# Kernel optimization log

Measured on AMD Instinct MI355X. Metric: run time of the kernel, lower is better.

The kernel has to match this reference:

```python
import jax, jax.numpy as jnp
import numpy as np

# TT-factorized linear: 784 = 7*4*7*4 -> 512 = 4*4*8*4, max_rank=20
# canonical TT ranks: [1, 20, 20, 16, 1] (r3 capped by m4*n4 = 16)
B = 16384
R1, R2, R3 = 20, 20, 16


def setup_inputs() -> dict:
    key = jax.random.key(0)
    k = jax.random.split(key, 6)
    x = jax.random.normal(k[0], (B, 784), jnp.float32)
    # TT cores G_k[r_{k-1}, m_k, n_k, r_k] with boundary ranks squeezed
    core1 = jax.random.normal(k[1], (7, 4, R1), jnp.float32) * 0.3   # [m1,n1,r1]
    core2 = jax.random.normal(k[2], (R1, 4, 4, R2), jnp.float32) * 0.1  # [r1,m2,n2,r2]
    core3 = jax.random.normal(k[3], (R2, 7, 8, R3), jnp.float32) * 0.05  # [r2,m3,n3,r3]
    core4 = jax.random.normal(k[4], (R3, 4, 4), jnp.float32) * 0.1   # [r3,m4,n4]
    bias = jax.random.normal(k[5], (512,), jnp.float32) * 0.01
    return {"x": x, "core1": core1, "core2": core2, "core3": core3,
            "core4": core4, "bias": bias}


def reference(x, core1, core2, core3, core4, bias):
    b = x.shape[0]
    # reshape input into TT mode factorization [B, m1, m2, m3, m4]
    x5 = x.reshape(b, 7, 4, 7, 4)
    # chain of small core contractions (the fusion-opportunity op pattern)
    t = jnp.einsum('bijkl,ipr->bjklpr', x5, core1)   # [B,4,7,4, n1,r1]
    t = jnp.einsum('bjklpr,rjqs->bklpqs', t, core2)  # [B,7,4, n1,n2,r2]
    t = jnp.einsum('bklpqs,sket->blpqet', t, core3)  # [B,4, n1,n2,n3,r3]
    y = jnp.einsum('blpqet,tlf->bpqef', t, core4)    # [B, n1,n2,n3,n4]
    y = y.reshape(b, 512) + bias
    # original forward: relu then softmax over features.
    # NOTE: the source calls self.fc2(y) but discards the result, so it is
    # omitted here (no effect on output).
    return jax.nn.softmax(jax.nn.relu(y), axis=1)
```

## Files before the change

### kernel.cpp

```cpp
#include <hip/hip_runtime.h>


typedef __attribute__((ext_vector_type(8))) short short8;
typedef __attribute__((ext_vector_type(4))) float floatx4;

__device__ __forceinline__ unsigned int pack2_bf16(float a, float b) {
    unsigned int ua = __float_as_uint(a);
    unsigned int ub = __float_as_uint(b);
    return ((ub + 0x8000u) & 0xFFFF0000u) | ((ua + 0x8000u) >> 16);
}

__device__ __forceinline__ short f32_to_bf16_rne(float v) {
    unsigned int u = __float_as_uint(v);
    return (short)(((u + 0x7FFFu + ((u >> 16) & 1)) >> 16) & 0xFFFF);
}

__global__ void prep_all(const float* __restrict__ c1, const float* __restrict__ c2,
                         const float* __restrict__ c3, const float* __restrict__ c4,
                         short* __restrict__ wp) {
    const int tid = threadIdx.x;
    const int blk = blockIdx.x;
    if (blk == 224) {
        for (int e = tid; e < 8192; e += 256) {
            int j   = e & 7;
            int lid = (e >> 3) & 15;
            int q2  = (e >> 7) & 1;
            int tn  = e >> 8;
            wp[(((tn * 25 + 24) * 64 + (2 + q2) * 16 + lid) << 3) + j] = 0;
        }
        return;
    }
    __shared__ float t12s[320];
    __shared__ float t123s[7 * 256];
    __shared__ float c4s[256];

    const int ij    = blk >> 3;
    const int strip = blk & 7;
    const int i  = ij >> 2, j2 = ij & 3;
    const int p  = strip >> 1;
    const int qh = strip & 1;

    if (tid < 256) c4s[tid] = c4[tid];
    for (int e = tid; e < 320; e += 256) {
        int s = e % 20, pq = e / 20;
        int pp = pq >> 2, q = pq & 3;
        float acc = 0.f;
        #pragma unroll
        for (int r = 0; r < 20; ++r)
            acc += c1[i * 80 + pp * 20 + r] * c2[r * 320 + j2 * 80 + q * 20 + s];
        t12s[e] = acc;
    }
    __syncthreads();

    for (int e = tid; e < 1792; e += 256) {
        int k3 = e >> 8, li = e & 255;
        int t = li & 15, pql = li >> 4;
        int qloc = pql >> 3, e3 = pql & 7;
        int q = 2 * qh + qloc;
        float acc = 0.f;
        const float* tp = t12s + (p * 4 + q) * 20;
        const float* cp = c3 + k3 * 128 + e3 * 16 + t;
        #pragma unroll
        for (int s = 0; s < 20; ++s) acc += tp[s] * cp[s * 896];
        t123s[e] = acc;
    }
    __syncthreads();

    for (int e = tid; e < 1792; e += 256) {
        int kl = e >> 6, nl = e & 63;
        int k = ij * 28 + kl;
        int n = strip * 64 + nl;
        int k3 = kl >> 2, l = kl & 3;
        int f4 = n & 3, e3 = (n >> 2) & 7;
        int pql = ((n >> 5) & 1) * 8 + e3;
        const float* tp = t123s + k3 * 256 + pql * 16;
        const float* cq = c4s + l * 4 + f4;
        float a = 0.f;
        #pragma unroll
        for (int t = 0; t < 16; ++t) a += tp[t] * cq[t * 16];
        int tk = k >> 5, quad = (k >> 3) & 3, j = k & 7;
        int tn = n >> 4, lid = n & 15;
        wp[(((tn * 25 + tk) * 64 + quad * 16 + lid) << 3) + j] = f32_to_bf16_rne(a);
    }
}

__global__ __launch_bounds__(512, 2) void tt_gemm(const float* __restrict__ x,
                                                  const short* __restrict__ wp,
                                                  const float* __restrict__ bias,
                                                  float* __restrict__ out) {
    __shared__ __align__(16) short s_a[6400 * 8];
    __shared__ float part[8][64];

    const int tid  = threadIdx.x;
    const int w    = tid >> 6;
    const int lane = tid & 63;
    const int quad = lane >> 4;
    const int lid  = lane & 15;
    const int m_base = blockIdx.x * 64;

    const short* wpw = wp + ((size_t)(w * 4) * 25 * 64 + lane) * 8;

    short8 b_f[3][4];
    #pragma unroll
    for (int nt = 0; nt < 4; ++nt) {
        b_f[0][nt] = *(const short8*)(wpw + (size_t)(nt * 25 + 0) * 64 * 8);
        b_f[1][nt] = *(const short8*)(wpw + (size_t)(nt * 25 + 1) * 64 * 8);
    }

    floatx4 h0[4], h1[4];
    #pragma unroll
    for (int i = 0; i < 4; ++i) {
        h0[i] = floatx4{0.f, 0.f, 0.f, 0.f};
        h1[i] = floatx4{0.f, 0.f, 0.f, 0.f};
        const int c = 4608 + tid + i * 512;
        if (c < 6400) {
            const int row = ((c >> 6) & 3) * 16 + (c & 15);
            const int kc  = ((c >> 8) * 4 + ((c >> 4) & 3)) * 8;
            if (kc < 784) {
                const floatx4* pp = (const floatx4*)(x + (size_t)(m_base + row) * 784 + kc);
                h0[i] = pp[0]; h1[i] = pp[1];
            }
        }
    }

    #pragma unroll
    for (int it = 0; it < 9; ++it) {
        const int a   = tid + it * 512;
        const int row = ((a >> 6) & 3) * 16 + (a & 15);
        const int kc  = ((a >> 8) * 4 + ((a >> 4) & 3)) * 8;
        const floatx4* pp = (const floatx4*)(x + (size_t)(m_base + row) * 784 + kc);
        floatx4 v0 = pp[0], v1 = pp[1];
        union { short8 s; unsigned int u[4]; } af;
        af.u[0] = pack2_bf16(v0.x, v0.y);
        af.u[1] = pack2_bf16(v0.z, v0.w);
        af.u[2] = pack2_bf16(v1.x, v1.y);
        af.u[3] = pack2_bf16(v1.z, v1.w);
        *(short8*)&s_a[a * 8] = af.s;
    }
    __syncthreads();

    const short* sa = s_a + lane * 8;

    floatx4 acc[4][4];
    #pragma unroll
    for (int mt = 0; mt < 4; ++mt)
        #pragma unroll
        for (int nt = 0; nt < 4; ++nt)
            acc[mt][nt] = floatx4{0.f, 0.f, 0.f, 0.f};

    short8 a_f[2][4];
    #pragma unroll
    for (int mt = 0; mt < 4; ++mt)
        a_f[0][mt] = *(const short8*)(sa + (size_t)(mt * 64) * 8);

    #pragma unroll
    for (int tk = 0; tk < 18; ++tk) {
        #pragma unroll
        for (int nt = 0; nt < 4; ++nt)
            b_f[(tk + 2) % 3][nt] = *(const short8*)(wpw + (size_t)(nt * 25 + tk + 2) * 64 * 8);
        if (tk + 1 < 18) {
            const short* sa2 = sa + (size_t)(tk + 1) * 256 * 8;
            #pragma unroll
            for (int mt = 0; mt < 4; ++mt)
                a_f[(tk + 1) & 1][mt] = *(const short8*)(sa2 + (size_t)(mt * 64) * 8);
        }
        #pragma unroll
        for (int nt = 0; nt < 4; ++nt)
            #pragma unroll
            for (int mt = 0; mt < 4; ++mt)
                acc[mt][nt] = __builtin_amdgcn_mfma_f32_16x16x32_bf16(a_f[tk & 1][mt], b_f[tk % 3][nt], acc[mt][nt], 0, 0, 0);
    }

    #pragma unroll
    for (int i = 0; i < 4; ++i) {
        const int c = 4608 + tid + i * 512;
        if (c < 6400) {
            union { short8 s; unsigned int u[4]; } af;
            af.u[0] = pack2_bf16(h0[i].x, h0[i].y);
            af.u[1] = pack2_bf16(h0[i].z, h0[i].w);
            af.u[2] = pack2_bf16(h1[i].x, h1[i].y);
            af.u[3] = pack2_bf16(h1[i].z, h1[i].w);
            *(short8*)&s_a[c * 8] = af.s;
        }
    }
    __syncthreads();

    #pragma unroll
    for (int mt = 0; mt < 4; ++mt)
        a_f[0][mt] = *(const short8*)(sa + ((size_t)18 * 256 + mt * 64) * 8);

    #pragma unroll
    for (int tk = 18; tk < 25; ++tk) {
        if (tk + 2 < 25) {
            #pragma unroll
            for (int nt = 0; nt < 4; ++nt)
                b_f[(tk + 2) % 3][nt] = *(const short8*)(wpw + (size_t)(nt * 25 + tk + 2) * 64 * 8);
        }
        if (tk + 1 < 25) {
            const short* sa2 = sa + (size_t)(tk + 1) * 256 * 8;
            #pragma unroll
            for (int mt = 0; mt < 4; ++mt)
                a_f[(tk + 1) & 1][mt] = *(const short8*)(sa2 + (size_t)(mt * 64) * 8);
        }
        #pragma unroll
        for (int nt = 0; nt < 4; ++nt)
            #pragma unroll
            for (int mt = 0; mt < 4; ++mt)
                acc[mt][nt] = __builtin_amdgcn_mfma_f32_16x16x32_bf16(a_f[tk & 1][mt], b_f[tk % 3][nt], acc[mt][nt], 0, 0, 0);
    }

    float bias_v[4];
    #pragma unroll
    for (int nt = 0; nt < 4; ++nt)
        bias_v[nt] = bias[w * 64 + nt * 16 + lid];

    #pragma unroll
    for (int mt = 0; mt < 4; ++mt) {
        #pragma unroll
        for (int reg = 0; reg < 4; ++reg) {
            float s = 0.f;
            #pragma unroll
            for (int nt = 0; nt < 4; ++nt) {
                float v = acc[mt][nt][reg] + bias_v[nt];
                v = fmaxf(v, 0.f);
                float e = __expf(v);
                acc[mt][nt][reg] = e;
                s += e;
            }
            s += __shfl_xor(s, 1, 64);
            s += __shfl_xor(s, 2, 64);
            s += __shfl_xor(s, 4, 64);
            s += __shfl_xor(s, 8, 64);
            if (lid == 0) part[w][mt * 16 + quad * 4 + reg] = s;
        }
    }
    __syncthreads();

    #pragma unroll
    for (int mt = 0; mt < 4; ++mt) {
        #pragma unroll
        for (int reg = 0; reg < 4; ++reg) {
            const int row = mt * 16 + quad * 4 + reg;
            float tot = 0.f;
            #pragma unroll
            for (int ww = 0; ww < 8; ++ww) tot += part[ww][row];
            const float inv = 1.0f / tot;
            #pragma unroll
            for (int nt = 0; nt < 4; ++nt)
                out[(size_t)(m_base + row) * 512 + w * 64 + nt * 16 + lid] = acc[mt][nt][reg] * inv;
        }
    }
}

extern "C" void kernel_launch(void* const* d_in, const int* in_sizes, int n_in,
                              void* d_out, int out_size, void* d_ws, size_t ws_size,
                              hipStream_t stream) {
    const float* x    = (const float*)d_in[0];
    const float* c1   = (const float*)d_in[1];
    const float* c2   = (const float*)d_in[2];
    const float* c3   = (const float*)d_in[3];
    const float* c4   = (const float*)d_in[4];
    const float* bias = (const float*)d_in[5];
    float* out = (float*)d_out;
    short* wpb = (short*)d_ws;

    prep_all<<<225, 256, 0, stream>>>(c1, c2, c3, c4, wpb);
    tt_gemm <<<256, 512, 0, stream>>>(x, wpb, bias, out);
}
```

Measured before the change: 125.3 us.

## Fuse weight prep and GEMM into one cooperative kernel with grid sync

Merges the TT-core weight-building kernel and the bf16 MFMA GEMM into a single cooperative launch. Within each block, waves 0-3 stage the x tile into LDS while waves 4-7 compute that block's slice of the packed weight matrix, then a grid-wide sync makes the full weights visible before the GEMM. This removes the second kernel launch and the gap between launches, and overlaps x staging with weight construction. In exchange it adds a grid barrier and threadfence, needs all 256 blocks co-resident, raises LDS use per block, and drops the earlier split staging that overlapped loading the x tail with the first MFMA steps.

```diff
diff --git a/kernel.cpp b/kernel.cpp
--- a/kernel.cpp
+++ b/kernel.cpp
@@ -1,4 +1,7 @@
 #include <hip/hip_runtime.h>
+#include <hip/hip_cooperative_groups.h>
+
+namespace cg = cooperative_groups;
 
 
 typedef __attribute__((ext_vector_type(8))) short short8;
@@ -15,24 +18,29 @@
     return (short)(((u + 0x7FFFu + ((u >> 16) & 1)) >> 16) & 0xFFFF);
 }
 
-__global__ void prep_all(const float* __restrict__ c1, const float* __restrict__ c2,
-                         const float* __restrict__ c3, const float* __restrict__ c4,
-                         short* __restrict__ wp) {
-    const int tid = threadIdx.x;
-    const int blk = blockIdx.x;
-    if (blk == 224) {
-        for (int e = tid; e < 8192; e += 256) {
-            int j   = e & 7;
-            int lid = (e >> 3) & 15;
-            int q2  = (e >> 7) & 1;
-            int tn  = e >> 8;
-            wp[(((tn * 25 + 24) * 64 + (2 + q2) * 16 + lid) << 3) + j] = 0;
-        }
-        return;
-    }
+__global__ __launch_bounds__(512, 2) void tt_fused(
+    const float* __restrict__ x,
+    const float* __restrict__ c1, const float* __restrict__ c2,
+    const float* __restrict__ c3, const float* __restrict__ c4,
+    const float* __restrict__ bias,
+    short* __restrict__ wp,
+    float* __restrict__ out)
+{
+    __shared__ __align__(16) short s_a[6400 * 8];
+    __shared__ float part[8][64];
     __shared__ float t12s[320];
     __shared__ float t123s[7 * 256];
     __shared__ float c4s[256];
+
+    const int tid  = threadIdx.x;
+    const int blk  = blockIdx.x;
+    const int w    = tid >> 6;
+    const int lane = tid & 63;
+    const int quad = lane >> 4;
+    const int lid  = lane & 15;
+    const int m_base = blk * 64;
+    const bool stager = (w < 4);
+    const int tp = tid & 255;
 
     const int ij    = blk >> 3;
     const int strip = blk & 7;
@@ -40,63 +48,119 @@
     const int p  = strip >> 1;
     const int qh = strip & 1;
 
-    if (tid < 256) c4s[tid] = c4[tid];
-    for (int e = tid; e < 320; e += 256) {
-        int s = e % 20, pq = e / 20;
-        int pp = pq >> 2, q = pq & 3;
-        float acc = 0.f;
-        #pragma unroll
-        for (int r = 0; r < 20; ++r)
-            acc += c1[i * 80 + pp * 20 + r] * c2[r * 320 + j2 * 80 + q * 20 + s];
-        t12s[e] = acc;
+    if (stager) {
+        #pragma unroll
+        for (int it = 0; it < 9; ++it) {
+            const int a   = tp + it * 256;
+            const int row = ((a >> 6) & 3) * 16 + (a & 15);
+            const int kc  = ((a >> 8) * 4 + ((a >> 4) & 3)) * 8;
+            floatx4 v0 = {0.f,0.f,0.f,0.f}, v1 = {0.f,0.f,0.f,0.f};
+            if (kc < 784) {
+                const floatx4* pp = (const floatx4*)(x + (size_t)(m_base + row) * 784 + kc);
+                v0 = pp[0]; v1 = pp[1];
+            }
+            union { short8 s; unsigned int u[4]; } af;
+            af.u[0] = pack2_bf16(v0.x, v0.y);
+            af.u[1] = pack2_bf16(v0.z, v0.w);
+            af.u[2] = pack2_bf16(v1.x, v1.y);
+            af.u[3] = pack2_bf16(v1.z, v1.w);
+            *(short8*)&s_a[a * 8] = af.s;
+        }
+    } else if (blk < 224) {
+        c4s[tp] = c4[tp];
+        for (int e = tp; e < 320; e += 256) {
+            int s = e % 20, pq = e / 20;
+            int pp_ = pq >> 2, q = pq & 3;
+            float acc = 0.f;
+            #pragma unroll
+            for (int r = 0; r < 20; ++r)
+                acc += c1[i * 80 + pp_ * 20 + r] * c2[r * 320 + j2 * 80 + q * 20 + s];
+            t12s[e] = acc;
+        }
     }
     __syncthreads();
 
-    for (int e = tid; e < 1792; e += 256) {
-        int k3 = e >> 8, li = e & 255;
-        int t = li & 15, pql = li >> 4;
-        int qloc = pql >> 3, e3 = pql & 7;
-        int q = 2 * qh + qloc;
-        float acc = 0.f;
-        const float* tp = t12s + (p * 4 + q) * 20;
-        const float* cp = c3 + k3 * 128 + e3 * 16 + t;
-        #pragma unroll
-        for (int s = 0; s < 20; ++s) acc += tp[s] * cp[s * 896];
-        t123s[e] = acc;
+    if (stager) {
+        #pragma unroll
+        for (int it = 9; it < 17; ++it) {
+            const int a   = tp + it * 256;
+            const int row = ((a >> 6) & 3) * 16 + (a & 15);
+            const int kc  = ((a >> 8) * 4 + ((a >> 4) & 3)) * 8;
+            floatx4 v0 = {0.f,0.f,0.f,0.f}, v1 = {0.f,0.f,0.f,0.f};
+            if (kc < 784) {
+                const floatx4* pp = (const floatx4*)(x + (size_t)(m_base + row) * 784 + kc);
+                v0 = pp[0]; v1 = pp[1];
+            }
+            union { short8 s; unsigned int u[4]; } af;
+            af.u[0] = pack2_bf16(v0.x, v0.y);
+            af.u[1] = pack2_bf16(v0.z, v0.w);
+            af.u[2] = pack2_bf16(v1.x, v1.y);
+            af.u[3] = pack2_bf16(v1.z, v1.w);
+            *(short8*)&s_a[a * 8] = af.s;
+        }
+    } else if (blk < 224) {
+        for (int e = tp; e < 1792; e += 256) {
+            int k3 = e >> 8, li = e & 255;
+            int t = li & 15, pql = li >> 4;
+            int qloc = pql >> 3, e3 = pql & 7;
+            int q = 2 * qh + qloc;
+            float acc = 0.f;
+            const float* tpt = t12s + (p * 4 + q) * 20;
+            const float* cp  = c3 + k3 * 128 + e3 * 16 + t;
+            #pragma unroll
+            for (int s = 0; s < 20; ++s) acc += tpt[s] * cp[s * 896];
+            t123s[e] = acc;
+        }
     }
     __syncthreads();
 
-    for (int e = tid; e < 1792; e += 256) {
-        int kl = e >> 6, nl = e & 63;
-        int k = ij * 28 + kl;
-        int n = strip * 64 + nl;
-        int k3 = kl >> 2, l = kl & 3;
-        int f4 = n & 3, e3 = (n >> 2) & 7;
-        int pql = ((n >> 5) & 1) * 8 + e3;
-        const float* tp = t123s + k3 * 256 + pql * 16;
-        const float* cq = c4s + l * 4 + f4;
-        float a = 0.f;
-        #pragma unroll
-        for (int t = 0; t < 16; ++t) a += tp[t] * cq[t * 16];
-        int tk = k >> 5, quad = (k >> 3) & 3, j = k & 7;
-        int tn = n >> 4, lid = n & 15;
-        wp[(((tn * 25 + tk) * 64 + quad * 16 + lid) << 3) + j] = f32_to_bf16_rne(a);
-    }
-}
-
-__global__ __launch_bounds__(512, 2) void tt_gemm(const float* __restrict__ x,
-                                                  const short* __restrict__ wp,
-                                                  const float* __restrict__ bias,
-                                                  float* __restrict__ out) {
-    __shared__ __align__(16) short s_a[6400 * 8];
-    __shared__ float part[8][64];
-
-    const int tid  = threadIdx.x;
-    const int w    = tid >> 6;
-    const int lane = tid & 63;
-    const int quad = lane >> 4;
-    const int lid  = lane & 15;
-    const int m_base = blockIdx.x * 64;
+    if (stager) {
+        #pragma unroll
+        for (int it = 17; it < 25; ++it) {
+            const int a   = tp + it * 256;
+            const int row = ((a >> 6) & 3) * 16 + (a & 15);
+            const int kc  = ((a >> 8) * 4 + ((a >> 4) & 3)) * 8;
+            floatx4 v0 = {0.f,0.f,0.f,0.f}, v1 = {0.f,0.f,0.f,0.f};
+            if (kc < 784) {
+                const floatx4* pp = (const floatx4*)(x + (size_t)(m_base + row) * 784 + kc);
+                v0 = pp[0]; v1 = pp[1];
+            }
+            union { short8 s; unsigned int u[4]; } af;
+            af.u[0] = pack2_bf16(v0.x, v0.y);
+            af.u[1] = pack2_bf16(v0.z, v0.w);
+            af.u[2] = pack2_bf16(v1.x, v1.y);
+            af.u[3] = pack2_bf16(v1.z, v1.w);
+            *(short8*)&s_a[a * 8] = af.s;
+        }
+    } else if (blk < 224) {
+        for (int e = tp; e < 1792; e += 256) {
+            int kl = e >> 6, nl = e & 63;
+            int k = ij * 28 + kl;
+            int n = strip * 64 + nl;
+            int k3 = kl >> 2, l = kl & 3;
+            int f4 = n & 3, e3 = (n >> 2) & 7;
+            int pql = ((n >> 5) & 1) * 8 + e3;
+            const float* tpt = t123s + k3 * 256 + pql * 16;
+            const float* cq  = c4s + l * 4 + f4;
+            float a = 0.f;
+            #pragma unroll
+            for (int t = 0; t < 16; ++t) a += tpt[t] * cq[t * 16];
+            int tk = k >> 5, q4 = (k >> 3) & 3, j = k & 7;
+            int tn = n >> 4, nlid = n & 15;
+            wp[(((tn * 25 + tk) * 64 + q4 * 16 + nlid) << 3) + j] = f32_to_bf16_rne(a);
+        }
+    } else if (blk == 224) {
+        for (int e = tp; e < 8192; e += 256) {
+            int j   = e & 7;
+            int nlid = (e >> 3) & 15;
+            int q2  = (e >> 7) & 1;
+            int tn  = e >> 8;
+            wp[(((tn * 25 + 24) * 64 + (2 + q2) * 16 + nlid) << 3) + j] = 0;
+        }
+    }
+
+    __threadfence();
+    cg::this_grid().sync();
 
     const short* wpw = wp + ((size_t)(w * 4) * 25 * 64 + lane) * 8;
 
@@ -107,38 +171,6 @@
         b_f[1][nt] = *(const short8*)(wpw + (size_t)(nt * 25 + 1) * 64 * 8);
     }
 
-    floatx4 h0[4], h1[4];
-    #pragma unroll
-    for (int i = 0; i < 4; ++i) {
-        h0[i] = floatx4{0.f, 0.f, 0.f, 0.f};
-        h1[i] = floatx4{0.f, 0.f, 0.f, 0.f};
-        const int c = 4608 + tid + i * 512;
-        if (c < 6400) {
-            const int row = ((c >> 6) & 3) * 16 + (c & 15);
-            const int kc  = ((c >> 8) * 4 + ((c >> 4) & 3)) * 8;
-            if (kc < 784) {
-                const floatx4* pp = (const floatx4*)(x + (size_t)(m_base + row) * 784 + kc);
-                h0[i] = pp[0]; h1[i] = pp[1];
-            }
-        }
-    }
-
-    #pragma unroll
-    for (int it = 0; it < 9; ++it) {
-        const int a   = tid + it * 512;
-        const int row = ((a >> 6) & 3) * 16 + (a & 15);
-        const int kc  = ((a >> 8) * 4 + ((a >> 4) & 3)) * 8;
-        const floatx4* pp = (const floatx4*)(x + (size_t)(m_base + row) * 784 + kc);
-        floatx4 v0 = pp[0], v1 = pp[1];
-        union { short8 s; unsigned int u[4]; } af;
-        af.u[0] = pack2_bf16(v0.x, v0.y);
-        af.u[1] = pack2_bf16(v0.z, v0.w);
-        af.u[2] = pack2_bf16(v1.x, v1.y);
-        af.u[3] = pack2_bf16(v1.z, v1.w);
-        *(short8*)&s_a[a * 8] = af.s;
-    }
-    __syncthreads();
-
     const short* sa = s_a + lane * 8;
 
     floatx4 acc[4][4];
@@ -154,43 +186,7 @@
         a_f[0][mt] = *(const short8*)(sa + (size_t)(mt * 64) * 8);
 
     #pragma unroll
-    for (int tk = 0; tk < 18; ++tk) {
-        #pragma unroll
-        for (int nt = 0; nt < 4; ++nt)
-            b_f[(tk + 2) % 3][nt] = *(const short8*)(wpw + (size_t)(nt * 25 + tk + 2) * 64 * 8);
-        if (tk + 1 < 18) {
-            const short* sa2 = sa + (size_t)(tk + 1) * 256 * 8;
-            #pragma unroll
-            for (int mt = 0; mt < 4; ++mt)
-                a_f[(tk + 1) & 1][mt] = *(const short8*)(sa2 + (size_t)(mt * 64) * 8);
-        }
-        #pragma unroll
-        for (int nt = 0; nt < 4; ++nt)
-            #pragma unroll
-            for (int mt = 0; mt < 4; ++mt)
-                acc[mt][nt] = __builtin_amdgcn_mfma_f32_16x16x32_bf16(a_f[tk & 1][mt], b_f[tk % 3][nt], acc[mt][nt], 0, 0, 0);
-    }
-
-    #pragma unroll
-    for (int i = 0; i < 4; ++i) {
-        const int c = 4608 + tid + i * 512;
-        if (c < 6400) {
-            union { short8 s; unsigned int u[4]; } af;
-            af.u[0] = pack2_bf16(h0[i].x, h0[i].y);
-            af.u[1] = pack2_bf16(h0[i].z, h0[i].w);
-            af.u[2] = pack2_bf16(h1[i].x, h1[i].y);
-            af.u[3] = pack2_bf16(h1[i].z, h1[i].w);
-            *(short8*)&s_a[c * 8] = af.s;
-        }
-    }
-    __syncthreads();
-
-    #pragma unroll
-    for (int mt = 0; mt < 4; ++mt)
-        a_f[0][mt] = *(const short8*)(sa + ((size_t)18 * 256 + mt * 64) * 8);
-
-    #pragma unroll
-    for (int tk = 18; tk < 25; ++tk) {
+    for (int tk = 0; tk < 25; ++tk) {
         if (tk + 2 < 25) {
             #pragma unroll
             for (int nt = 0; nt < 4; ++nt)
@@ -264,6 +260,8 @@
     float* out = (float*)d_out;
     short* wpb = (short*)d_ws;
 
-    prep_all<<<225, 256, 0, stream>>>(c1, c2, c3, c4, wpb);
-    tt_gemm <<<256, 512, 0, stream>>>(x, wpb, bias, out);
-}
+    void* args[] = {(void*)&x, (void*)&c1, (void*)&c2, (void*)&c3,
+                    (void*)&c4, (void*)&bias, (void*)&wpb, (void*)&out};
+    hipLaunchCooperativeKernel(reinterpret_cast<void*>(&tt_fused),
+                               dim3(256), dim3(512), args, 0, stream);
+}
```

After: 235.0 us. 1.88x slower.
